# Performance work log

Measured on AMD Instinct MI355X. Metric: run time of the kernel, lower is better.

The kernel has to match this reference:

```python
import jax, jax.numpy as jnp
import numpy as np
import math


def _dct2_mat(N):
    # DCT-II matrix, norm=None convention of torch_dct: X[k] = 2*sum_n x[n]*cos(pi*(2n+1)*k/(2N))
    n = np.arange(N)
    k = n[:, None]
    C = 2.0 * np.cos(np.pi * (2 * n[None, :] + 1) * k / (2 * N))
    return jnp.asarray(C, dtype=jnp.float32)


def setup_inputs() -> dict:
    key = jax.random.key(0)
    k1, k2, k3 = jax.random.split(key, 3)
    B, H, W = 128, 256, 256
    thresh = int(H / (2 * math.sqrt(2)))  # 90
    x = jax.random.normal(k1, (B, 3, H, W), dtype=jnp.float32)
    w = jax.random.normal(k2, (1, thresh), dtype=jnp.float32) * 0.05
    b = jax.random.normal(k3, (1,), dtype=jnp.float32) * 0.05
    return {"x": x, "w": w, "b": b}


def reference(x, w, b):
    B, C, H, W = x.shape
    Ch = _dct2_mat(H)
    Cw = _dct2_mat(W)
    # dct_2d: DCT-II along last two dims
    xd = jnp.einsum('bchw,kw->bchk', x, Cw)
    xd = jnp.einsum('bchk,jh->bcjk', xd, Ch)
    xd = jax.lax.stop_gradient(xd)  # original does x.detach() inside get_fft_feature
    gray = 0.2989 * xd[:, 0] + 0.587 * xd[:, 1] + 0.114 * xd[:, 2]  # [B,H,W]
    F = jnp.fft.fft2(gray, axes=(-2, -1))
    re = F.real + 1e-8  # original adds epsilon to both real and imag parts
    im = F.imag + 1e-8
    mag = jnp.log(jnp.sqrt(re * re + im * im + 1e-10) + 1e-10)
    mag = jnp.fft.fftshift(mag, axes=(-2, -1))  # quadrant-swap `shift` == fftshift for even dims
    # radial binning (static integer radii, as in azimuthalAverage)
    yy, xx = np.indices([H, W])
    r = np.sqrt((xx - H / 2) ** 2 + (yy - W / 2) ** 2).astype(np.int32).ravel()
    nbins = int(r.max()) + 1
    nr = jnp.asarray(np.bincount(r, minlength=nbins).astype(np.float32))
    rj = jnp.asarray(r)
    tbin = jax.vmap(lambda m: jax.ops.segment_sum(m, rj, num_segments=nbins))(mag.reshape(B, -1))
    prof = tbin / (nr + 1e-10)  # [B, nbins]
    prof = prof[:, 1:-2]  # azimuthalAverage returns radial_prof[1:-2]
    mn = jnp.min(prof, axis=1, keepdims=True)
    mx = jnp.max(prof, axis=1, keepdims=True)
    out = (prof - mn) / (mx - mn)
    out = jnp.where(jnp.isnan(out), 0.0, out)
    thresh = w.shape[1]
    feat = out[:, -thresh:]  # [B, thresh]
    return feat @ w.T + b  # [B, 1]
```

## Files before the change

kernel.cpp:

```cpp
#include <hip/hip_runtime.h>
#include <math.h>

#define NBINS 182
#define NB 128

typedef unsigned short u16;
typedef __attribute__((ext_vector_type(8))) short short8;
typedef __attribute__((ext_vector_type(4))) float f32x4;

__device__ __forceinline__ u16 f2bf(float f) {
    union { float f; unsigned u; } v; v.f = f;
    unsigned r = v.u + 0x7FFF + ((v.u >> 16) & 1);
    return (u16)(r >> 16);
}
__device__ __forceinline__ float bf2f(u16 u) {
    union { unsigned u; float f; } v; v.u = ((unsigned)u) << 16;
    return v.f;
}
__device__ __forceinline__ short8 negbf(short8 v) {
    short8 r;
#pragma unroll
    for (int i = 0; i < 8; ++i) r[i] = v[i] ^ (short)0x8000;
    return r;
}

__device__ __forceinline__ int radial_bin(int dx, int dy) {
    int d2 = dx * dx + dy * dy;
    int bin = (int)sqrtf((float)d2);
    while ((bin + 1) * (bin + 1) <= d2) ++bin;
    while (bin * bin > d2) --bin;
    return bin;
}

__global__ __launch_bounds__(256) void prep(const float* __restrict__ x,
                                            u16* __restrict__ G,
                                            float* __restrict__ M_re,
                                            float* __restrict__ M_im,
                                            u16* __restrict__ A1,
                                            float* __restrict__ nrpart,
                                            float* __restrict__ tbin,
                                            u16* __restrict__ Tt_im) {
    __shared__ double ctab[1024];
    __shared__ double stab[1024];
    __shared__ float s[NBINS];
    int blk = blockIdx.x;
    int t = threadIdx.x;

    if (blk < 256) {
        for (int i = t; i < 1024; i += 256) {
            double a = 3.14159265358979323846 * (double)i / 512.0;
            ctab[i] = cos(a);
            stab[i] = sin(a);
        }
        __syncthreads();
        int j = blk;
        int w = t;
        double re = 0.0, im = 0.0;
        int tw = 2 * w + 1;
        for (int k = 0; k < 256; ++k) {
            int e = (4 * j * k) & 1023;
            int m = (tw * k) & 1023;
            double cw = 2.0 * ctab[m];
            re += ctab[e] * cw;
            im -= stab[e] * cw;
        }
        M_re[j * 256 + w] = (float)re;
        M_im[j * 256 + w] = (float)im;
        A1[j * 256 + w] = f2bf((float)re);
        A1[(j + 256) * 256 + w] = f2bf((float)im);
    } else if (blk < 512) {
        int i = blk - 256;
        if (t < NBINS) s[t] = 0.0f;
        __syncthreads();
        int bin = radial_bin(t - 128, i - 128);
        atomicAdd(&s[bin], 1.0f);
        __syncthreads();
        if (t < NBINS) nrpart[i * NBINS + t] = s[t];
    } else if (blk < 544) {
        int idx = (blk - 512) * 256 + t;
        for (int i = idx; i < NB * NBINS; i += 32 * 256) tbin[i] = 0.0f;
        for (int i = idx; i < NB * 128; i += 32 * 256) {
            int bb = i >> 7, off = (i & 127) << 1;
            *(unsigned*)(Tt_im + (size_t)bb * 65536 + 128 * 256 + off) = 0u;
        }
    } else {
        int tid = (blk - 544) * 256 + t;
        for (int i = tid; i < 2097152; i += 262144) {
            int idx = i * 4;
            int b = idx >> 16;
            int rem = idx & 65535;
            const float* p = x + (size_t)b * 196608 + rem;
            float4 r = *(const float4*)p;
            float4 g = *(const float4*)(p + 65536);
            float4 bl = *(const float4*)(p + 131072);
            float g0 = 0.2989f * r.x + 0.587f * g.x + 0.114f * bl.x;
            float g1 = 0.2989f * r.y + 0.587f * g.y + 0.114f * bl.y;
            float g2 = 0.2989f * r.z + 0.587f * g.z + 0.114f * bl.z;
            float g3 = 0.2989f * r.w + 0.587f * g.w + 0.114f * bl.w;
            uint2 o;
            o.x = (unsigned)f2bf(g0) | ((unsigned)f2bf(g1) << 16);
            o.y = (unsigned)f2bf(g2) | ((unsigned)f2bf(g3) << 16);
            *(uint2*)(G + idx) = o;
        }
    }
}

__global__ __launch_bounds__(256) void s1(const u16* __restrict__ A1,
                                          const u16* __restrict__ G,
                                          u16* __restrict__ Tt_re,
                                          u16* __restrict__ Tt_im) {
    int b = blockIdx.z;
    int t = threadIdx.x;

    if (blockIdx.y == 2) {
        int lane = t & 63, wv = t >> 6;
        int fr = lane & 15;
        int fk = (lane >> 4) << 3;
        const u16* Ap = A1 + (size_t)(128 + fr) * 256;
        const u16* Gb = G + (size_t)b * 65536;
        int c0 = blockIdx.x * 128 + wv * 32;
        f32x4 acc[2];
        acc[0] = (f32x4){0.f, 0.f, 0.f, 0.f};
        acc[1] = (f32x4){0.f, 0.f, 0.f, 0.f};
        for (int kk = 0; kk < 256; kk += 32) {
            short8 af = *(const short8*)(Ap + kk + fk);
#pragma unroll
            for (int sub = 0; sub < 2; ++sub) {
                short8 bfv = *(const short8*)(Gb + (size_t)(c0 + sub * 16 + fr) * 256 + kk + fk);
                acc[sub] = __builtin_amdgcn_mfma_f32_16x16x32_bf16(
                    af, bfv, acc[sub], 0, 0, 0);
            }
        }
        if ((lane >> 4) == 0) {
            size_t base = (size_t)b * 65536 + 128 * 256;
            Tt_re[base + c0 + lane] = f2bf(acc[0][0]);
            Tt_re[base + c0 + 16 + lane] = f2bf(acc[1][0]);
        }
        return;
    }

    __shared__ u16 As[128 * 40];
    __shared__ u16 Bs[128 * 40];
    int r0 = blockIdx.y * 256;
    int h0 = blockIdx.x * 128;
    int lane = t & 63, wv = t >> 6;
    int wr = (wv >> 1) * 64;
    int wc = (wv & 1) * 64;
    int fr = lane & 15;
    int fk = (lane >> 4) << 3;

    f32x4 acc[4][4];
#pragma unroll
    for (int i = 0; i < 4; ++i)
#pragma unroll
        for (int j = 0; j < 4; ++j) acc[i][j] = (f32x4){0.f, 0.f, 0.f, 0.f};

    const u16* Ap = A1 + (size_t)r0 * 256;
    const u16* Gp = G + (size_t)b * 65536 + (size_t)h0 * 256;

    for (int kk = 0; kk < 256; kk += 32) {
#pragma unroll
        for (int c = t; c < 512; c += 256) {
            int row = c >> 2, off = (c & 3) << 3;
            *(uint4*)&As[row * 40 + off] =
                *(const uint4*)(Ap + (size_t)row * 256 + kk + off);
            *(uint4*)&Bs[row * 40 + off] =
                *(const uint4*)(Gp + (size_t)row * 256 + kk + off);
        }
        __syncthreads();
        short8 af[4], bfr[4];
#pragma unroll
        for (int i = 0; i < 4; ++i)
            af[i] = *(const short8*)&As[(wr + i * 16 + fr) * 40 + fk];
#pragma unroll
        for (int j = 0; j < 4; ++j)
            bfr[j] = *(const short8*)&Bs[(wc + j * 16 + fr) * 40 + fk];
#pragma unroll
        for (int i = 0; i < 4; ++i)
#pragma unroll
            for (int j = 0; j < 4; ++j)
                acc[i][j] = __builtin_amdgcn_mfma_f32_16x16x32_bf16(
                    af[i], bfr[j], acc[i][j], 0, 0, 0);
        __syncthreads();
    }

    u16* dst = ((r0 < 256) ? Tt_re : Tt_im) + (size_t)b * 65536;
    int rq = (lane >> 4) << 2;
#pragma unroll
    for (int i = 0; i < 4; ++i)
#pragma unroll
        for (int j = 0; j < 4; ++j) {
            int col = h0 + wc + j * 16 + fr;
#pragma unroll
            for (int reg = 0; reg < 4; ++reg) {
                int row = wr + i * 16 + rq + reg;
                dst[(size_t)row * 256 + col] = f2bf(acc[i][j][reg]);
            }
        }
}

__global__ __launch_bounds__(256) void s2f(const u16* __restrict__ A1,
                                           const float* __restrict__ M_re,
                                           const u16* __restrict__ Tt_re,
                                           const u16* __restrict__ Tt_im,
                                           float* __restrict__ tbin) {
    __shared__ u16 Ar[64 * 40], Ai[64 * 40], Br[64 * 40], Bi[64 * 40];
    __shared__ u16 Br3[16 * 40], Bi3[16 * 40];
    __shared__ float sbins[NBINS];
    __shared__ float sM[256];
    int blk = blockIdx.x;
    int t = threadIdx.x;

    if (blk >= 512) {
        int b = blk - 512;
        sM[t] = M_re[128 * 256 + t];
        __syncthreads();
        if (t > 128) return;
        const u16* pr = Tt_re + (size_t)b * 65536 + (size_t)t * 256;
        const u16* pi = Tt_im + (size_t)b * 65536 + (size_t)t * 256;
        float re = 0.0f, im = 0.0f;
        for (int h = 0; h < 256; h += 8) {
            uint4 vr = *(const uint4*)(pr + h);
            uint4 vi = *(const uint4*)(pi + h);
            unsigned wr[4] = {vr.x, vr.y, vr.z, vr.w};
            unsigned wi[4] = {vi.x, vi.y, vi.z, vi.w};
#pragma unroll
            for (int q = 0; q < 4; ++q) {
                re = fmaf(sM[h + 2 * q], bf2f((u16)(wr[q] & 0xffff)), re);
                re = fmaf(sM[h + 2 * q + 1], bf2f((u16)(wr[q] >> 16)), re);
                im = fmaf(sM[h + 2 * q], bf2f((u16)(wi[q] & 0xffff)), im);
                im = fmaf(sM[h + 2 * q + 1], bf2f((u16)(wi[q] >> 16)), im);
            }
        }
        re += 1e-8f; im += 1e-8f;
        float mag = logf(sqrtf(re * re + im * im + 1e-10f) + 1e-10f);
        float wj = (t == 0 || t == 128) ? 1.0f : 2.0f;
        int dx = (t < 128) ? t : t - 256;
        int bin = radial_bin(dx, -128);
        atomicAdd(&tbin[b * NBINS + bin], wj * mag);
        return;
    }

    int b = blk >> 2;
    int u0 = ((blk >> 1) & 1) * 64;
    int j0 = (blk & 1) * 64;
    int lane = t & 63, wv = t >> 6;
    int wu = (wv >> 1) * 32;
    int wj = (wv & 1) * 32;
    int fr = lane & 15;
    int fk = (lane >> 4) << 3;
    bool do128 = (j0 == 64) && ((wv & 1) == 0);

    for (int i = t; i < NBINS; i += 256) sbins[i] = 0.0f;

    f32x4 accr1[2][2], acci1[2][2], accr2[2][2], acci2[2][2];
    f32x4 acc3r[2], acc3i[2];
#pragma unroll
    for (int i = 0; i < 2; ++i) {
#pragma unroll
        for (int j = 0; j < 2; ++j) {
            accr1[i][j] = (f32x4){0.f, 0.f, 0.f, 0.f};
            acci1[i][j] = (f32x4){0.f, 0.f, 0.f, 0.f};
            accr2[i][j] = (f32x4){0.f, 0.f, 0.f, 0.f};
            acci2[i][j] = (f32x4){0.f, 0.f, 0.f, 0.f};
        }
        acc3r[i] = (f32x4){0.f, 0.f, 0.f, 0.f};
        acc3i[i] = (f32x4){0.f, 0.f, 0.f, 0.f};
    }

    const u16* Apr = A1 + (size_t)u0 * 256;
    const u16* Api = A1 + (size_t)(256 + u0) * 256;

    int lrow = t >> 2, loff = (t & 3) << 3;
    const u16* Trs = Tt_re + (size_t)b * 65536 + (size_t)(j0 + lrow) * 256;
    const u16* Tis = Tt_im + (size_t)b * 65536 + (size_t)(j0 + lrow) * 256;
    int r3 = (t & 63) >> 2, o3 = (t & 3) << 3;
    const u16* T3s = (((t >> 6) == 0) ? Tt_re : Tt_im)
                   + (size_t)b * 65536 + (size_t)(128 + r3) * 256;

    for (int kk = 0; kk < 256; kk += 32) {
        *(uint4*)&Ar[lrow * 40 + loff] =
            *(const uint4*)(Apr + (size_t)lrow * 256 + kk + loff);
        *(uint4*)&Ai[lrow * 40 + loff] =
            *(const uint4*)(Api + (size_t)lrow * 256 + kk + loff);
        *(uint4*)&Br[lrow * 40 + loff] = *(const uint4*)(Trs + kk + loff);
        *(uint4*)&Bi[lrow * 40 + loff] = *(const uint4*)(Tis + kk + loff);
        if (j0 == 64 && t < 128) {
            uint4 v3 = *(const uint4*)(T3s + kk + o3);
            if (t < 64) *(uint4*)&Br3[r3 * 40 + o3] = v3;
            else        *(uint4*)&Bi3[r3 * 40 + o3] = v3;
        }
        __syncthreads();
        short8 arf[2], aif[2], naif[2], brf[2], bif[2], nbif[2];
#pragma unroll
        for (int i = 0; i < 2; ++i) {
            arf[i] = *(const short8*)&Ar[(wu + i * 16 + fr) * 40 + fk];
            aif[i] = *(const short8*)&Ai[(wu + i * 16 + fr) * 40 + fk];
            naif[i] = negbf(aif[i]);
        }
#pragma unroll
        for (int j = 0; j < 2; ++j) {
            brf[j] = *(const short8*)&Br[(wj + j * 16 + fr) * 40 + fk];
            bif[j] = *(const short8*)&Bi[(wj + j * 16 + fr) * 40 + fk];
            nbif[j] = negbf(bif[j]);
        }
#pragma unroll
        for (int i = 0; i < 2; ++i)
#pragma unroll
            for (int j = 0; j < 2; ++j) {
                accr1[i][j] = __builtin_amdgcn_mfma_f32_16x16x32_bf16(
                    arf[i], brf[j], accr1[i][j], 0, 0, 0);
                accr1[i][j] = __builtin_amdgcn_mfma_f32_16x16x32_bf16(
                    naif[i], bif[j], accr1[i][j], 0, 0, 0);
                acci1[i][j] = __builtin_amdgcn_mfma_f32_16x16x32_bf16(
                    arf[i], bif[j], acci1[i][j], 0, 0, 0);
                acci1[i][j] = __builtin_amdgcn_mfma_f32_16x16x32_bf16(
                    aif[i], brf[j], acci1[i][j], 0, 0, 0);
                accr2[i][j] = __builtin_amdgcn_mfma_f32_16x16x32_bf16(
                    arf[i], brf[j], accr2[i][j], 0, 0, 0);
                accr2[i][j] = __builtin_amdgcn_mfma_f32_16x16x32_bf16(
                    aif[i], bif[j], accr2[i][j], 0, 0, 0);
                acci2[i][j] = __builtin_amdgcn_mfma_f32_16x16x32_bf16(
                    arf[i], nbif[j], acci2[i][j], 0, 0, 0);
                acci2[i][j] = __builtin_amdgcn_mfma_f32_16x16x32_bf16(
                    aif[i], brf[j], acci2[i][j], 0, 0, 0);
            }
        if (do128) {
            short8 brf3 = *(const short8*)&Br3[fr * 40 + fk];
            short8 bif3 = *(const short8*)&Bi3[fr * 40 + fk];
#pragma unroll
            for (int i = 0; i < 2; ++i) {
                acc3r[i] = __builtin_amdgcn_mfma_f32_16x16x32_bf16(
                    arf[i], brf3, acc3r[i], 0, 0, 0);
                acc3r[i] = __builtin_amdgcn_mfma_f32_16x16x32_bf16(
                    naif[i], bif3, acc3r[i], 0, 0, 0);
                acc3i[i] = __builtin_amdgcn_mfma_f32_16x16x32_bf16(
                    arf[i], bif3, acc3i[i], 0, 0, 0);
                acc3i[i] = __builtin_amdgcn_mfma_f32_16x16x32_bf16(
                    aif[i], brf3, acc3i[i], 0, 0, 0);
            }
        }
        __syncthreads();
    }

    int rq = (lane >> 4) << 2;
#pragma unroll
    for (int i = 0; i < 2; ++i)
#pragma unroll
        for (int j = 0; j < 2; ++j) {
            int v = j0 + wj + j * 16 + fr;
#pragma unroll
            for (int reg = 0; reg < 4; ++reg) {
                int u = u0 + wu + i * 16 + rq + reg;
                float wrow = (u == 0) ? 1.0f : 2.0f;
                float re1 = accr1[i][j][reg] + 1e-8f;
                float im1 = acci1[i][j][reg] + 1e-8f;
                float m1 = logf(sqrtf(re1 * re1 + im1 * im1 + 1e-10f) + 1e-10f);
                float val;
                if (v == 0) {
                    val = wrow * m1;
                } else {
                    float re2 = accr2[i][j][reg] + 1e-8f;
                    float im2 = acci2[i][j][reg] + 1e-8f;
                    float m2 = logf(sqrtf(re2 * re2 + im2 * im2 + 1e-10f) + 1e-10f);
                    val = wrow * (m1 + m2);
                }
                int bin = radial_bin(v, u);
                atomicAdd(&sbins[bin], val);
            }
        }
    if (do128 && fr == 0) {
#pragma unroll
        for (int i = 0; i < 2; ++i)
#pragma unroll
            for (int reg = 0; reg < 4; ++reg) {
                int u = u0 + wu + i * 16 + rq + reg;
                float wrow = (u == 0) ? 1.0f : 2.0f;
                float re = acc3r[i][reg] + 1e-8f;
                float im = acc3i[i][reg] + 1e-8f;
                float mag = logf(sqrtf(re * re + im * im + 1e-10f) + 1e-10f);
                int bin = radial_bin(-128, u);
                atomicAdd(&sbins[bin], wrow * mag);
            }
    }
    __syncthreads();
    for (int i = t; i < NBINS; i += 256)
        atomicAdd(&tbin[b * NBINS + i], sbins[i]);
}

__global__ __launch_bounds__(192) void finalize(const float* __restrict__ tbin,
                                                const float* __restrict__ nrpart,
                                                const float* __restrict__ w,
                                                const float* __restrict__ bias,
                                                float* __restrict__ out) {
    __shared__ float prof[NBINS];
    __shared__ float smn, smx, ssum;
    int b = blockIdx.x;
    int t = threadIdx.x;
    if (t < NBINS) {
        float nr = 0.0f;
        for (int i = 0; i < 256; ++i) nr += nrpart[i * NBINS + t];
        prof[t] = tbin[b * NBINS + t] / (nr + 1e-10f);
    }
    __syncthreads();
    if (t == 0) {
        float mn = prof[1], mx = prof[1];
        for (int i = 2; i <= 179; ++i) {
            float p = prof[i];
            mn = fminf(mn, p);
            mx = fmaxf(mx, p);
        }
        smn = mn; smx = mx; ssum = 0.0f;
    }
    __syncthreads();
    if (t < 90) {
        float denom = smx - smn;
        float v = (prof[90 + t] - smn) / denom;
        if (v != v) v = 0.0f;
        atomicAdd(&ssum, v * w[t]);
    }
    __syncthreads();
    if (t == 0) out[b] = ssum + bias[0];
}

extern "C" void kernel_launch(void* const* d_in, const int* in_sizes, int n_in,
                              void* d_out, int out_size, void* d_ws, size_t ws_size,
                              hipStream_t stream) {
    const float* x = (const float*)d_in[0];
    const float* w = (const float*)d_in[1];
    const float* bias = (const float*)d_in[2];
    float* out = (float*)d_out;

    float* M_re = (float*)d_ws;
    float* M_im = M_re + 65536;
    u16* A1 = (u16*)(M_im + 65536);
    u16* G = A1 + 131072;
    u16* Tt_re = G + (size_t)NB * 65536;
    u16* Tt_im = Tt_re + (size_t)NB * 65536;
    float* tbin = (float*)(Tt_im + (size_t)NB * 65536);
    float* nrpart = tbin + NB * NBINS;

    prep<<<1568, 256, 0, stream>>>(x, G, M_re, M_im, A1, nrpart, tbin, Tt_im);
    s1<<<dim3(2, 3, NB), 256, 0, stream>>>(A1, G, Tt_re, Tt_im);
    s2f<<<640, 256, 0, stream>>>(A1, M_re, Tt_re, Tt_im, tbin);
    finalize<<<NB, 192, 0, stream>>>(tbin, nrpart, w, bias, out);
}
```

Measured before the change: 208.5 us.

## Restructure s1 GEMM to register-direct MFMA with folded row-128 computation

The first-stage GEMM drops its LDS-staged 128x128 tiles and the separate row-128 block. Each 512-thread block now handles 32 output rows across re and im. Waves load A and G fragments straight from global memory into MFMA operands, and q==0 blocks fold in the row-128 vector product. This removes shared-memory traffic, barriers and the extra special-case blocks, at the cost of uncoalesced global fragment loads and redundant reads of G across blocks, which rely on L2. The s2f MFMA calls are only rewritten with a macro.

```diff
diff --git a/kernel.cpp b/kernel.cpp
--- a/kernel.cpp
+++ b/kernel.cpp
@@ -31,6 +31,8 @@
     while (bin * bin > d2) --bin;
     return bin;
 }
+
+#define MFMA __builtin_amdgcn_mfma_f32_16x16x32_bf16
 
 __global__ __launch_bounds__(256) void prep(const float* __restrict__ x,
                                             u16* __restrict__ G,
@@ -105,98 +107,57 @@
     }
 }
 
-__global__ __launch_bounds__(256) void s1(const u16* __restrict__ A1,
+__global__ __launch_bounds__(512) void s1(const u16* __restrict__ A1,
                                           const u16* __restrict__ G,
                                           u16* __restrict__ Tt_re,
                                           u16* __restrict__ Tt_im) {
     int b = blockIdx.z;
+    int q = blockIdx.x;
     int t = threadIdx.x;
-
-    if (blockIdx.y == 2) {
-        int lane = t & 63, wv = t >> 6;
-        int fr = lane & 15;
-        int fk = (lane >> 4) << 3;
-        const u16* Ap = A1 + (size_t)(128 + fr) * 256;
-        const u16* Gb = G + (size_t)b * 65536;
-        int c0 = blockIdx.x * 128 + wv * 32;
-        f32x4 acc[2];
-        acc[0] = (f32x4){0.f, 0.f, 0.f, 0.f};
-        acc[1] = (f32x4){0.f, 0.f, 0.f, 0.f};
-        for (int kk = 0; kk < 256; kk += 32) {
-            short8 af = *(const short8*)(Ap + kk + fk);
-#pragma unroll
-            for (int sub = 0; sub < 2; ++sub) {
-                short8 bfv = *(const short8*)(Gb + (size_t)(c0 + sub * 16 + fr) * 256 + kk + fk);
-                acc[sub] = __builtin_amdgcn_mfma_f32_16x16x32_bf16(
-                    af, bfv, acc[sub], 0, 0, 0);
-            }
-        }
-        if ((lane >> 4) == 0) {
-            size_t base = (size_t)b * 65536 + 128 * 256;
-            Tt_re[base + c0 + lane] = f2bf(acc[0][0]);
-            Tt_re[base + c0 + 16 + lane] = f2bf(acc[1][0]);
-        }
-        return;
-    }
-
-    __shared__ u16 As[128 * 40];
-    __shared__ u16 Bs[128 * 40];
-    int r0 = blockIdx.y * 256;
-    int h0 = blockIdx.x * 128;
     int lane = t & 63, wv = t >> 6;
-    int wr = (wv >> 1) * 64;
-    int wc = (wv & 1) * 64;
     int fr = lane & 15;
     int fk = (lane >> 4) << 3;
-
-    f32x4 acc[4][4];
-#pragma unroll
-    for (int i = 0; i < 4; ++i)
-#pragma unroll
-        for (int j = 0; j < 4; ++j) acc[i][j] = (f32x4){0.f, 0.f, 0.f, 0.f};
-
-    const u16* Ap = A1 + (size_t)r0 * 256;
-    const u16* Gp = G + (size_t)b * 65536 + (size_t)h0 * 256;
+    int rq = (lane >> 4) << 2;
+    int tau = wv & 3, hh = wv >> 2;
+    int arow = (tau < 2) ? (32 * q + 16 * tau) : (256 + 32 * q + 16 * (tau - 2));
+
+    const u16* Af = A1 + (size_t)(arow + fr) * 256;
+    const u16* A28 = A1 + (size_t)(128 + fr) * 256;
+    const u16* Gb = G + (size_t)b * 65536;
+
+    f32x4 acc[8], a128[2];
+#pragma unroll
+    for (int j = 0; j < 8; ++j) acc[j] = (f32x4){0.f, 0.f, 0.f, 0.f};
+    a128[0] = (f32x4){0.f, 0.f, 0.f, 0.f};
+    a128[1] = (f32x4){0.f, 0.f, 0.f, 0.f};
 
     for (int kk = 0; kk < 256; kk += 32) {
-#pragma unroll
-        for (int c = t; c < 512; c += 256) {
-            int row = c >> 2, off = (c & 3) << 3;
-            *(uint4*)&As[row * 40 + off] =
-                *(const uint4*)(Ap + (size_t)row * 256 + kk + off);
-            *(uint4*)&Bs[row * 40 + off] =
-                *(const uint4*)(Gp + (size_t)row * 256 + kk + off);
-        }
-        __syncthreads();
-        short8 af[4], bfr[4];
-#pragma unroll
-        for (int i = 0; i < 4; ++i)
-            af[i] = *(const short8*)&As[(wr + i * 16 + fr) * 40 + fk];
-#pragma unroll
-        for (int j = 0; j < 4; ++j)
-            bfr[j] = *(const short8*)&Bs[(wc + j * 16 + fr) * 40 + fk];
-#pragma unroll
-        for (int i = 0; i < 4; ++i)
-#pragma unroll
-            for (int j = 0; j < 4; ++j)
-                acc[i][j] = __builtin_amdgcn_mfma_f32_16x16x32_bf16(
-                    af[i], bfr[j], acc[i][j], 0, 0, 0);
-        __syncthreads();
-    }
-
-    u16* dst = ((r0 < 256) ? Tt_re : Tt_im) + (size_t)b * 65536;
-    int rq = (lane >> 4) << 2;
-#pragma unroll
-    for (int i = 0; i < 4; ++i)
-#pragma unroll
-        for (int j = 0; j < 4; ++j) {
-            int col = h0 + wc + j * 16 + fr;
-#pragma unroll
-            for (int reg = 0; reg < 4; ++reg) {
-                int row = wr + i * 16 + rq + reg;
-                dst[(size_t)row * 256 + col] = f2bf(acc[i][j][reg]);
-            }
-        }
+        short8 afr = *(const short8*)(Af + kk + fk);
+        short8 a28f = *(const short8*)(A28 + kk + fk);
+#pragma unroll
+        for (int j2 = 0; j2 < 8; ++j2) {
+            int j = 8 * hh + j2;
+            short8 bf = *(const short8*)(Gb + (size_t)(16 * j + fr) * 256 + kk + fk);
+            acc[j2] = MFMA(afr, bf, acc[j2], 0, 0, 0);
+            if (q == 0 && (j >> 1) == wv)
+                a128[j & 1] = MFMA(a28f, bf, a128[j & 1], 0, 0, 0);
+        }
+    }
+
+    u16* dst = ((tau < 2) ? Tt_re : Tt_im) + (size_t)b * 65536;
+    int orow = 32 * q + 16 * (tau & 1);
+#pragma unroll
+    for (int j2 = 0; j2 < 8; ++j2) {
+        int col = 16 * (8 * hh + j2) + fr;
+#pragma unroll
+        for (int reg = 0; reg < 4; ++reg)
+            dst[(size_t)(orow + rq + reg) * 256 + col] = f2bf(acc[j2][reg]);
+    }
+    if (q == 0 && (lane >> 4) == 0) {
+        size_t base = (size_t)b * 65536 + 128 * 256;
+        Tt_re[base + 32 * wv + lane] = f2bf(a128[0][0]);
+        Tt_re[base + 32 * wv + 16 + lane] = f2bf(a128[1][0]);
+    }
 }
 
 __global__ __launch_bounds__(256) void s2f(const u16* __restrict__ A1,
@@ -308,36 +269,24 @@
         for (int i = 0; i < 2; ++i)
 #pragma unroll
             for (int j = 0; j < 2; ++j) {
-                accr1[i][j] = __builtin_amdgcn_mfma_f32_16x16x32_bf16(
-                    arf[i], brf[j], accr1[i][j], 0, 0, 0);
-                accr1[i][j] = __builtin_amdgcn_mfma_f32_16x16x32_bf16(
-                    naif[i], bif[j], accr1[i][j], 0, 0, 0);
-                acci1[i][j] = __builtin_amdgcn_mfma_f32_16x16x32_bf16(
-                    arf[i], bif[j], acci1[i][j], 0, 0, 0);
-                acci1[i][j] = __builtin_amdgcn_mfma_f32_16x16x32_bf16(
-                    aif[i], brf[j], acci1[i][j], 0, 0, 0);
-                accr2[i][j] = __builtin_amdgcn_mfma_f32_16x16x32_bf16(
-                    arf[i], brf[j], accr2[i][j], 0, 0, 0);
-                accr2[i][j] = __builtin_amdgcn_mfma_f32_16x16x32_bf16(
-                    aif[i], bif[j], accr2[i][j], 0, 0, 0);
-                acci2[i][j] = __builtin_amdgcn_mfma_f32_16x16x32_bf16(
-                    arf[i], nbif[j], acci2[i][j], 0, 0, 0);
-                acci2[i][j] = __builtin_amdgcn_mfma_f32_16x16x32_bf16(
-                    aif[i], brf[j], acci2[i][j], 0, 0, 0);
+                accr1[i][j] = MFMA(arf[i], brf[j], accr1[i][j], 0, 0, 0);
+                accr1[i][j] = MFMA(naif[i], bif[j], accr1[i][j], 0, 0, 0);
+                acci1[i][j] = MFMA(arf[i], bif[j], acci1[i][j], 0, 0, 0);
+                acci1[i][j] = MFMA(aif[i], brf[j], acci1[i][j], 0, 0, 0);
+                accr2[i][j] = MFMA(arf[i], brf[j], accr2[i][j], 0, 0, 0);
+                accr2[i][j] = MFMA(aif[i], bif[j], accr2[i][j], 0, 0, 0);
+                acci2[i][j] = MFMA(arf[i], nbif[j], acci2[i][j], 0, 0, 0);
+                acci2[i][j] = MFMA(aif[i], brf[j], acci2[i][j], 0, 0, 0);
             }
         if (do128) {
             short8 brf3 = *(const short8*)&Br3[fr * 40 + fk];
             short8 bif3 = *(const short8*)&Bi3[fr * 40 + fk];
 #pragma unroll
             for (int i = 0; i < 2; ++i) {
-                acc3r[i] = __builtin_amdgcn_mfma_f32_16x16x32_bf16(
-                    arf[i], brf3, acc3r[i], 0, 0, 0);
-                acc3r[i] = __builtin_amdgcn_mfma_f32_16x16x32_bf16(
-                    naif[i], bif3, acc3r[i], 0, 0, 0);
-                acc3i[i] = __builtin_amdgcn_mfma_f32_16x16x32_bf16(
-                    arf[i], bif3, acc3i[i], 0, 0, 0);
-                acc3i[i] = __builtin_amdgcn_mfma_f32_16x16x32_bf16(
-                    aif[i], brf3, acc3i[i], 0, 0, 0);
+                acc3r[i] = MFMA(arf[i], brf3, acc3r[i], 0, 0, 0);
+                acc3r[i] = MFMA(naif[i], bif3, acc3r[i], 0, 0, 0);
+                acc3i[i] = MFMA(arf[i], bif3, acc3i[i], 0, 0, 0);
+                acc3i[i] = MFMA(aif[i], brf3, acc3i[i], 0, 0, 0);
             }
         }
         __syncthreads();
@@ -441,7 +390,7 @@
     float* nrpart = tbin + NB * NBINS;
 
     prep<<<1568, 256, 0, stream>>>(x, G, M_re, M_im, A1, nrpart, tbin, Tt_im);
-    s1<<<dim3(2, 3, NB), 256, 0, stream>>>(A1, G, Tt_re, Tt_im);
+    s1<<<dim3(4, 1, NB), 512, 0, stream>>>(A1, G, Tt_re, Tt_im);
     s2f<<<640, 256, 0, stream>>>(A1, M_re, Tt_re, Tt_im, tbin);
     finalize<<<NB, 192, 0, stream>>>(tbin, nrpart, w, bias, out);
 }
```

Result: slower. 233.4 us (+11.9%).
